# Kernel tuning notes

Measured on AMD Instinct MI355X. Metric: run time of the kernel, lower is better.

The kernel has to match this reference:

```python
import jax, jax.numpy as jnp
import numpy as np
from jax import lax

B, C, K = 16, 320, 8  # batch, channels, template kernel size
EPS = 1e-12  # F.normalize eps


def _pool_to(x, k):
    # adaptive avg pool to (k, k); H, W are exact multiples of k here
    b, c, h, w = x.shape
    return x.reshape(b, c, k, h // k, k, w // k).mean(axis=(3, 5))


def _l2norm(x):
    # L2 normalize over channel dim (dim=1), matching F.normalize(p=2, dim=1)
    n = jnp.sqrt(jnp.sum(x * x, axis=1, keepdims=True))
    return x / jnp.maximum(n, EPS)


def _fusion(feats, w1, b1, w2, b2):
    # global avg pool -> 2-layer MLP score per template -> softmax -> weighted sum
    scores = jnp.concatenate(
        [jax.nn.relu(f.mean(axis=(2, 3)) @ w1 + b1) @ w2 + b2 for f in feats], axis=1
    )  # (B, 3)
    a = jax.nn.softmax(scores, axis=1)
    return sum(a[:, i, None, None, None] * feats[i] for i in range(3))


def _corr(template_kernel, search):
    # depthwise correlation + channel sum == per-sample VALID conv with a
    # single (1, C, K, K) kernel; vmap over batch
    tn = _l2norm(template_kernel)  # (B, C, K, K)
    sn = _l2norm(search)           # (B, C, H, W)

    def one(sb, tb):
        return lax.conv_general_dilated(
            sb[None], tb[None], (1, 1), 'VALID',
            dimension_numbers=('NCHW', 'OIHW', 'NCHW'))[0]  # (1, Ho, Wo)

    return jax.vmap(one)(sn, tn)  # (B, 1, Ho, Wo)


_SPECS = [
    ('t0_p3', (B, C, 32, 32)), ('t0_p4', (B, C, 16, 16)), ('t0_p5', (B, C, 8, 8)),
    ('t1_p3', (B, C, 32, 32)), ('t1_p4', (B, C, 16, 16)), ('t1_p5', (B, C, 8, 8)),
    ('t2_p3', (B, C, 32, 32)), ('t2_p4', (B, C, 16, 16)), ('t2_p5', (B, C, 8, 8)),
    ('s_p3', (B, C, 64, 64)), ('s_p4', (B, C, 32, 32)), ('s_p5', (B, C, 16, 16)),
]
_PARAMS = [
    ('fp3_w1', (C, C // 4)), ('fp3_b1', (C // 4,)), ('fp3_w2', (C // 4, 1)), ('fp3_b2', (1,)),
    ('fp4_w1', (C, C // 4)), ('fp4_b1', (C // 4,)), ('fp4_w2', (C // 4, 1)), ('fp4_b2', (1,)),
    ('fp5_w1', (C, C // 4)), ('fp5_b1', (C // 4,)), ('fp5_w2', (C // 4, 1)), ('fp5_b2', (1,)),
]


def setup_inputs() -> dict:
    key = jax.random.key(0)
    d = {}
    for i, (name, shape) in enumerate(_SPECS):
        d[name] = jax.random.normal(jax.random.fold_in(key, i), shape, jnp.float32)
    for j, (name, shape) in enumerate(_PARAMS):
        k = jax.random.fold_in(key, 100 + j)
        if name.endswith('b1') or name.endswith('b2'):
            d[name] = jnp.zeros(shape, jnp.float32)
        else:
            d[name] = jax.random.normal(k, shape, jnp.float32) * 0.05
    return d


def reference(t0_p3, t0_p4, t0_p5, t1_p3, t1_p4, t1_p5, t2_p3, t2_p4, t2_p5,
              s_p3, s_p4, s_p5,
              fp3_w1, fp3_b1, fp3_w2, fp3_b2,
              fp4_w1, fp4_b1, fp4_w2, fp4_b2,
              fp5_w1, fp5_b1, fp5_w2, fp5_b2):
    tp3 = _fusion([t0_p3, t1_p3, t2_p3], fp3_w1, fp3_b1, fp3_w2, fp3_b2)
    tp4 = _fusion([t0_p4, t1_p4, t2_p4], fp4_w1, fp4_b1, fp4_w2, fp4_b2)
    tp5 = _fusion([t0_p5, t1_p5, t2_p5], fp5_w1, fp5_b1, fp5_w2, fp5_b2)
    corr_p3 = _corr(_pool_to(tp3, K), s_p3)  # (B, 1, 57, 57)
    corr_p4 = _corr(_pool_to(tp4, K), s_p4)  # (B, 1, 25, 25)
    corr_p5 = _corr(_pool_to(tp5, K), s_p5)  # (B, 1, 9, 9)
    return (corr_p3, corr_p4, corr_p5)
```

## Files before the change

### kernel.cpp

```cpp
#include <hip/hip_runtime.h>
#include <math.h>

#define BATCH 16
#define CH 320

typedef __attribute__((ext_vector_type(8))) short bf16x8;
typedef __attribute__((ext_vector_type(4))) float f32x4;

union FragU { bf16x8 f; unsigned long long u[2]; };

static constexpr size_t PLSZ     = (size_t)BATCH * CH * 64;
static constexpr size_t WS_POOL3 = 0;
static constexpr size_t WS_POOL4 = 3 * PLSZ;
static constexpr size_t WS_TF    = 6 * PLSZ;
static constexpr size_t WS_MEANS = 9 * PLSZ;
static constexpr size_t WS_AW    = WS_MEANS + 9 * BATCH * CH;
static constexpr size_t WS_PART  = WS_AW + 144;
static constexpr size_t WS_ABF   = WS_PART + 3 * BATCH * 80 * 64;
static constexpr size_t UB3 = 0;
static constexpr size_t UB4 = (size_t)BATCH * 4096 * 64;
static constexpr size_t UB5 = UB4 + (size_t)BATCH * 1024 * 64;

__device__ __forceinline__ float bf2f(unsigned short u) {
    union { unsigned int i; float f; } x; x.i = ((unsigned int)u) << 16; return x.f;
}
__device__ __forceinline__ unsigned short f2bf(float f) {
    union { float f; unsigned int i; } x; x.f = f;
    return (unsigned short)((x.i + 0x7FFFu + ((x.i >> 16) & 1u)) >> 16);
}
__device__ __forceinline__ unsigned cvtpk(float lo, float hi) {
    unsigned r;
    asm("v_cvt_pk_bf16_f32 %0, %1, %2" : "=v"(r) : "v"(lo), "v"(hi));
    return r;
}

template <int HW, int KK>
__device__ __forceinline__ void pool_body(int idx, const float* __restrict__ a0,
                                          const float* __restrict__ a1, const float* __restrict__ a2,
                                          float* __restrict__ dst, float* __restrict__ means, int lane) {
    constexpr int NPL = BATCH * CH * 64;
    int tmpl = idx / NPL;
    int r = idx % NPL;
    const float* src = (tmpl == 0) ? a0 : ((tmpl == 1) ? a1 : a2);
    int bc = r >> 6;
    int pos = r & 63;
    int oh = pos >> 3, ow = pos & 7;
    const float* base = src + (size_t)bc * HW * HW;
    float s = 0.0f;
    if constexpr (KK == 4) {
#pragma unroll
        for (int i = 0; i < 4; ++i) {
            float4 v = *(const float4*)(base + (oh * 4 + i) * HW + ow * 4);
            s += v.x + v.y + v.z + v.w;
        }
    } else {
#pragma unroll
        for (int i = 0; i < 2; ++i) {
            float2 v = *(const float2*)(base + (oh * 2 + i) * HW + ow * 2);
            s += v.x + v.y;
        }
    }
    s *= (1.0f / (KK * KK));
    dst[idx] = s;
    float m = s;
#pragma unroll
    for (int o = 32; o; o >>= 1) m += __shfl_xor(m, o);
    if (lane == 0) means[tmpl * (BATCH * CH) + bc] = m * (1.0f / 64.0f);
}

__global__ __launch_bounds__(256) void prep_kernel(
    const float* __restrict__ t0p3, const float* __restrict__ t1p3, const float* __restrict__ t2p3,
    const float* __restrict__ t0p4, const float* __restrict__ t1p4, const float* __restrict__ t2p4,
    const float* __restrict__ t0p5, const float* __restrict__ t1p5, const float* __restrict__ t2p5,
    float* __restrict__ pool3, float* __restrict__ pool4, float* __restrict__ means) {
    int bid = blockIdx.x, t = threadIdx.x, lane = t & 63;
    if (bid < 3840) {
        pool_body<32, 4>(bid * 256 + t, t0p3, t1p3, t2p3, pool3, means, lane);
    } else if (bid < 7680) {
        pool_body<16, 2>((bid - 3840) * 256 + t, t0p4, t1p4, t2p4, pool4, means + 3 * BATCH * CH, lane);
    } else {
        int w = ((bid - 7680) * 256 + t) >> 6;
        constexpr int NR = BATCH * CH;
        int tmpl = w / NR, rem = w % NR;
        const float* src = (tmpl == 0) ? t0p5 : ((tmpl == 1) ? t1p5 : t2p5);
        float v = src[(size_t)rem * 64 + lane];
#pragma unroll
        for (int o = 32; o; o >>= 1) v += __shfl_xor(v, o);
        if (lane == 0) means[6 * BATCH * CH + w] = v * (1.0f / 64.0f);
    }
}

__global__ __launch_bounds__(256) void weights_kernel(const float* __restrict__ means,
        const float* w13, const float* b13, const float* w23, const float* b23,
        const float* w14, const float* b14, const float* w24, const float* b24,
        const float* w15, const float* b15, const float* w25, const float* b25,
        float* __restrict__ a_out) {
    __shared__ float m[3 * CH];
    __shared__ float hv[240];
    __shared__ float sc[3];
    int lvl = blockIdx.x / BATCH;
    int b = blockIdx.x % BATCH;
    int t = threadIdx.x;
    const float* w1 = (lvl == 0) ? w13 : ((lvl == 1) ? w14 : w15);
    const float* b1 = (lvl == 0) ? b13 : ((lvl == 1) ? b14 : b15);
    const float* w2 = (lvl == 0) ? w23 : ((lvl == 1) ? w24 : w25);
    const float* b2 = (lvl == 0) ? b23 : ((lvl == 1) ? b24 : b25);
    const float* mb = means + lvl * (3 * BATCH * CH);
    for (int j = t; j < 3 * CH; j += 256) {
        int i = j / CH, c = j % CH;
        m[j] = mb[i * (BATCH * CH) + b * CH + c];
    }
    __syncthreads();
    if (t < 240) {
        int i = t / 80, jj = t % 80;
        float acc = b1[jj];
#pragma unroll 4
        for (int c = 0; c < CH; ++c) acc = fmaf(m[i * CH + c], w1[c * 80 + jj], acc);
        hv[t] = fmaxf(acc, 0.0f) * w2[jj];
    }
    __syncthreads();
    if (t < 3) {
        float s = b2[0];
#pragma unroll 8
        for (int jj = 0; jj < 80; ++jj) s += hv[t * 80 + jj];
        sc[t] = s;
    }
    __syncthreads();
    if (t == 0) {
        float mx = fmaxf(sc[0], fmaxf(sc[1], sc[2]));
        float e0 = expf(sc[0] - mx), e1 = expf(sc[1] - mx), e2 = expf(sc[2] - mx);
        float inv = 1.0f / (e0 + e1 + e2);
        float* ao = a_out + lvl * 48 + b * 3;
        ao[0] = e0 * inv; ao[1] = e1 * inv; ao[2] = e2 * inv;
    }
}

__global__ __launch_bounds__(256) void fuse_kernel(
        const float* __restrict__ p30, const float* __restrict__ p31, const float* __restrict__ p32,
        const float* __restrict__ p40, const float* __restrict__ p41, const float* __restrict__ p42,
        const float* __restrict__ p50, const float* __restrict__ p51, const float* __restrict__ p52,
        const float* __restrict__ aw, float* __restrict__ tf, float* __restrict__ partial) {
    __shared__ float red[256];
    int lvl = blockIdx.x / 1280;
    int r = blockIdx.x % 1280;
    int t = threadIdx.x;
    const float* p0 = (lvl == 0) ? p30 : ((lvl == 1) ? p40 : p50);
    const float* p1 = (lvl == 0) ? p31 : ((lvl == 1) ? p41 : p51);
    const float* p2 = (lvl == 0) ? p32 : ((lvl == 1) ? p42 : p52);
    int idx = r * 256 + t;
    int b = r / 80;
    int j = r % 80;
    const float* ab = aw + lvl * 48 + b * 3;
    float a0 = ab[0], a1 = ab[1], a2 = ab[2];
    float v = a0 * p0[idx] + a1 * p1[idx] + a2 * p2[idx];
    tf[(size_t)lvl * PLSZ + idx] = v;
    red[t] = v * v;
    __syncthreads();
    if (t < 64) {
        float s = red[t] + red[t + 64] + red[t + 128] + red[t + 192];
        partial[((size_t)(lvl * BATCH + b) * 80 + j) * 64 + t] = s;
    }
}

__global__ __launch_bounds__(256) void atrans_kernel(const float* __restrict__ tf,
        const float* __restrict__ part, short* __restrict__ abf) {
    __shared__ float lds[64 * 68];
    __shared__ float red2[4 * 64];
    __shared__ float sv[64];
    int lvl = blockIdx.x >> 4;
    int b = blockIdx.x & 15;
    int t = threadIdx.x;
    {
        const float* p = part + ((size_t)(lvl * BATCH + b) * 80) * 64 + (t & 63);
        int jg = t >> 6;
        float s = 0.0f;
        for (int j = jg * 20; j < jg * 20 + 20; ++j) s += p[j * 64];
        red2[jg * 64 + (t & 63)] = s;
    }
    __syncthreads();
    if (t < 64) {
        float s = red2[t] + red2[64 + t] + red2[128 + t] + red2[192 + t];
        sv[t] = 1.0f / fmaxf(sqrtf(s), 1e-12f);
    }
    __syncthreads();
    const float* tb = tf + (size_t)lvl * PLSZ + (size_t)b * (CH * 64);
    short* ab = abf + ((size_t)(lvl * BATCH + b) * 64) * 320;
    for (int c0 = 0; c0 < 320; c0 += 64) {
        __syncthreads();
#pragma unroll
        for (int i = 0; i < 4; ++i) {
            int c = (t >> 4) + 16 * i;
            int p4 = (t & 15) * 4;
            *(float4*)(lds + c * 68 + p4) = *(const float4*)(tb + (size_t)(c0 + c) * 64 + p4);
        }
        __syncthreads();
        int p = t >> 2;
        int cs = (t & 3) * 16;
        float s_p = sv[p];
        bf16x8 o0, o1;
#pragma unroll
        for (int u = 0; u < 8; ++u) o0[u] = (short)f2bf(lds[(cs + u) * 68 + p] * s_p);
#pragma unroll
        for (int u = 0; u < 8; ++u) o1[u] = (short)f2bf(lds[(cs + 8 + u) * 68 + p] * s_p);
        *(bf16x8*)(ab + (size_t)p * 320 + c0 + cs) = o0;
        *(bf16x8*)(ab + (size_t)p * 320 + c0 + cs + 8) = o1;
    }
}

template <int H>
__device__ __forceinline__ void gemm_body(const float* __restrict__ S, const short* __restrict__ T,
                                          short* __restrict__ V, int bid,
                                          unsigned short* St, float* red, float* invs) {
    constexpr int N = H * H;
    constexpr int XB = N / 64;
    int b = bid / XB;
    int x0b = (bid % XB) * 64;
    int t = threadIdx.x;
    int w = t >> 6, l = t & 63, g = l >> 4, ln = l & 15;
    int cg = t >> 4;
    int x0 = (t & 15) * 4;

    const float* Sb = S + (size_t)b * CH * N + x0b;
    const short* Tp = T + ((size_t)b * 64 + 16 * w + ln) * 320 + 8 * g;

    f32x4 acc[4];
#pragma unroll
    for (int i = 0; i < 4; ++i) acc[i] = (f32x4){0.f, 0.f, 0.f, 0.f};
    float ssq[4] = {0.f, 0.f, 0.f, 0.f};

    unsigned trbase = (unsigned)(size_t)St + (unsigned)(g * 256 + ln * 8);
    int e1 = ((x0 >> 4) * 8 + (cg >> 2)) * 64 + (cg & 3) * 16 + (x0 & 15);

    {
        const float* p = Sb + (size_t)cg * N + x0;
        float4 v1 = *(const float4*)(p);
        float4 v2 = *(const float4*)(p + (size_t)16 * N);
        ssq[0] = fmaf(v1.x, v1.x, fmaf(v2.x, v2.x, ssq[0]));
        ssq[1] = fmaf(v1.y, v1.y, fmaf(v2.y, v2.y, ssq[1]));
        ssq[2] = fmaf(v1.z, v1.z, fmaf(v2.z, v2.z, ssq[2]));
        ssq[3] = fmaf(v1.w, v1.w, fmaf(v2.w, v2.w, ssq[3]));
        *(uint2*)(St + e1)       = (uint2){cvtpk(v1.x, v1.y), cvtpk(v1.z, v1.w)};
        *(uint2*)(St + e1 + 256) = (uint2){cvtpk(v2.x, v2.y), cvtpk(v2.z, v2.w)};
    }
    bf16x8 tcur = *(const bf16x8*)(Tp);
    __syncthreads();

#define TRRD2(FR, OFF) \
    asm volatile("ds_read_b64_tr_b16 %0, %2 offset:%c3\n\tds_read_b64_tr_b16 %1, %2 offset:%c4" \
                 : "=v"((FR).u[0]), "=v"((FR).u[1]) : "v"(trbase), "i"(OFF), "i"((OFF) + 128));

#define GSTEP(BUF, S_) { \
    int kn = 32 * ((S_) + 1); \
    bool dost = kn < 320; \
    int kl = dost ? kn : 288; \
    const float* p_ = Sb + (size_t)(kl + cg) * N + x0; \
    float4 v1 = *(const float4*)(p_); \
    float4 v2 = *(const float4*)(p_ + (size_t)16 * N); \
    bf16x8 tnx = *(const bf16x8*)(Tp + kl); \
    FragU fr0, fr1, fr2, fr3; \
    TRRD2(fr0, (BUF) * 4096 + 0) \
    TRRD2(fr1, (BUF) * 4096 + 1024) \
    TRRD2(fr2, (BUF) * 4096 + 2048) \
    TRRD2(fr3, (BUF) * 4096 + 3072) \
    asm volatile("s_waitcnt lgkmcnt(0)" ::: "memory"); \
    __builtin_amdgcn_sched_barrier(0); \
    acc[0] = __builtin_amdgcn_mfma_f32_16x16x32_bf16(fr0.f, tcur, acc[0], 0, 0, 0); \
    acc[1] = __builtin_amdgcn_mfma_f32_16x16x32_bf16(fr1.f, tcur, acc[1], 0, 0, 0); \
    acc[2] = __builtin_amdgcn_mfma_f32_16x16x32_bf16(fr2.f, tcur, acc[2], 0, 0, 0); \
    acc[3] = __builtin_amdgcn_mfma_f32_16x16x32_bf16(fr3.f, tcur, acc[3], 0, 0, 0); \
    if (dost) { \
        ssq[0] = fmaf(v1.x, v1.x, fmaf(v2.x, v2.x, ssq[0])); \
        ssq[1] = fmaf(v1.y, v1.y, fmaf(v2.y, v2.y, ssq[1])); \
        ssq[2] = fmaf(v1.z, v1.z, fmaf(v2.z, v2.z, ssq[2])); \
        ssq[3] = fmaf(v1.w, v1.w, fmaf(v2.w, v2.w, ssq[3])); \
        unsigned short* d_ = St + (((BUF) ^ 1) * 2048) + e1; \
        *(uint2*)(d_)       = (uint2){cvtpk(v1.x, v1.y), cvtpk(v1.z, v1.w)}; \
        *(uint2*)(d_ + 256) = (uint2){cvtpk(v2.x, v2.y), cvtpk(v2.z, v2.w)}; \
    } \
    tcur = tnx; \
    __syncthreads(); }

    for (int s = 0; s < 10; s += 2) {
        GSTEP(0, s)
        GSTEP(1, s + 1)
    }
#undef GSTEP
#undef TRRD2

    *(f32x4*)(red + cg * 64 + x0) = (f32x4){ssq[0], ssq[1], ssq[2], ssq[3]};
    __syncthreads();
    if (t < 64) {
        float s = 0.0f;
#pragma unroll
        for (int i = 0; i < 16; ++i) s += red[i * 64 + t];
        invs[t] = 1.0f / fmaxf(sqrtf(s), 1e-12f);
    }
    __syncthreads();

    short* Vb = V + ((size_t)b * N + x0b) * 64 + 16 * w + ln;
#pragma unroll
    for (int mt = 0; mt < 4; ++mt) {
        f32x4 iv = *(f32x4*)(invs + mt * 16 + 4 * g);
#pragma unroll
        for (int r = 0; r < 4; ++r)
            Vb[(size_t)(mt * 16 + 4 * g + r) * 64] = (short)f2bf(acc[mt][r] * iv[r]);
    }
}

__global__ __launch_bounds__(256) void gemm_kernel(const float* __restrict__ sp3,
        const float* __restrict__ sp4, const float* __restrict__ sp5,
        const short* __restrict__ abf, short* __restrict__ u) {
    __shared__ unsigned short St[2 * 2048];
    __shared__ float red[16 * 64];
    __shared__ float invs[64];
    int bid = blockIdx.x;
    if (bid < 1024)      gemm_body<64>(sp3, abf,          u + UB3, bid,        St, red, invs);
    else if (bid < 1280) gemm_body<32>(sp4, abf + 327680, u + UB4, bid - 1024, St, red, invs);
    else                 gemm_body<16>(sp5, abf + 655360, u + UB5, bid - 1280, St, red, invs);
}

__global__ __launch_bounds__(256) void combine_kernel(const short* __restrict__ U,
                                                      float* __restrict__ out) {
    int tid = blockIdx.x * 256 + threadIdx.x;
    if (tid < 51984) {
        int b = tid / 3249, r = tid % 3249;
        int oh = r / 57, ow = r % 57;
        const short* u = U + UB3 + ((size_t)b * 4096 + oh * 64 + ow) * 64;
        float s = 0.0f;
#pragma unroll
        for (int kh = 0; kh < 8; ++kh)
#pragma unroll
            for (int kw = 0; kw < 8; ++kw)
                s += bf2f((unsigned short)u[(kh * 64 + kw) * 64 + kh * 8 + kw]);
        out[tid] = s;
    } else if (tid < 61984) {
        int x = tid - 51984;
        int b = x / 625, r = x % 625;
        int oh = r / 25, ow = r % 25;
        const short* u = U + UB4 + ((size_t)b * 1024 + oh * 32 + ow) * 64;
        float s = 0.0f;
#pragma unroll
        for (int kh = 0; kh < 8; ++kh)
#pragma unroll
            for (int kw = 0; kw < 8; ++kw)
                s += bf2f((unsigned short)u[(kh * 32 + kw) * 64 + kh * 8 + kw]);
        out[tid] = s;
    } else if (tid < 63280) {
        int x = tid - 61984;
        int b = x / 81, r = x % 81;
        int oh = r / 9, ow = r % 9;
        const short* u = U + UB5 + ((size_t)b * 256 + oh * 16 + ow) * 64;
        float s = 0.0f;
#pragma unroll
        for (int kh = 0; kh < 8; ++kh)
#pragma unroll
            for (int kw = 0; kw < 8; ++kw)
                s += bf2f((unsigned short)u[(kh * 16 + kw) * 64 + kh * 8 + kw]);
        out[tid] = s;
    }
}

extern "C" void kernel_launch(void* const* d_in, const int* in_sizes, int n_in,
                              void* d_out, int out_size, void* d_ws, size_t ws_size,
                              hipStream_t stream) {
    const float* t0p3 = (const float*)d_in[0];
    const float* t0p4 = (const float*)d_in[1];
    const float* t0p5 = (const float*)d_in[2];
    const float* t1p3 = (const float*)d_in[3];
    const float* t1p4 = (const float*)d_in[4];
    const float* t1p5 = (const float*)d_in[5];
    const float* t2p3 = (const float*)d_in[6];
    const float* t2p4 = (const float*)d_in[7];
    const float* t2p5 = (const float*)d_in[8];
    const float* sp3  = (const float*)d_in[9];
    const float* sp4  = (const float*)d_in[10];
    const float* sp5  = (const float*)d_in[11];
    const float* f3w1 = (const float*)d_in[12];
    const float* f3b1 = (const float*)d_in[13];
    const float* f3w2 = (const float*)d_in[14];
    const float* f3b2 = (const float*)d_in[15];
    const float* f4w1 = (const float*)d_in[16];
    const float* f4b1 = (const float*)d_in[17];
    const float* f4w2 = (const float*)d_in[18];
    const float* f4b2 = (const float*)d_in[19];
    const float* f5w1 = (const float*)d_in[20];
    const float* f5b1 = (const float*)d_in[21];
    const float* f5w2 = (const float*)d_in[22];
    const float* f5b2 = (const float*)d_in[23];

    float* ws = (float*)d_ws;
    short* abf = (short*)(ws + WS_ABF);
    short* ubuf = (short*)ws;

    prep_kernel<<<11520, 256, 0, stream>>>(t0p3, t1p3, t2p3, t0p4, t1p4, t2p4,
                                           t0p5, t1p5, t2p5,
                                           ws + WS_POOL3, ws + WS_POOL4, ws + WS_MEANS);
    weights_kernel<<<48, 256, 0, stream>>>(ws + WS_MEANS,
                                           f3w1, f3b1, f3w2, f3b2,
                                           f4w1, f4b1, f4w2, f4b2,
                                           f5w1, f5b1, f5w2, f5b2, ws + WS_AW);
    fuse_kernel<<<3840, 256, 0, stream>>>(ws + WS_POOL3, ws + WS_POOL3 + PLSZ, ws + WS_POOL3 + 2 * PLSZ,
                                          ws + WS_POOL4, ws + WS_POOL4 + PLSZ, ws + WS_POOL4 + 2 * PLSZ,
                                          t0p5, t1p5, t2p5,
                                          ws + WS_AW, ws + WS_TF, ws + WS_PART);
    atrans_kernel<<<48, 256, 0, stream>>>(ws + WS_TF, ws + WS_PART, abf);
    gemm_kernel<<<1344, 256, 0, stream>>>(sp3, sp4, sp5, abf, ubuf);
    combine_kernel<<<248, 256, 0, stream>>>(ubuf, (float*)d_out);
}
```

Before: 89.38 us.

## Deepen global prefetch to three stages in search GEMM and raise MFMA priority

The search-feature GEMM loop now keeps global loads three K-steps ahead in a register ring instead of one, fully unrolls the ten steps, and moves the LDS store of the next tile before the wait so it overlaps the fragment reads. It wraps the MFMA block in s_setprio and replaces __syncthreads with raw s_barrier after an explicit lgkmcnt wait. Launch bounds now request four waves per SIMD. The aim is to hide HBM latency in a memory-bound loop, at the cost of more registers, which the occupancy hint may force into spills.

```diff
diff --git a/kernel.cpp b/kernel.cpp
--- a/kernel.cpp
+++ b/kernel.cpp
@@ -213,6 +213,8 @@
                                           unsigned short* St, float* red, float* invs) {
     constexpr int N = H * H;
     constexpr int XB = N / 64;
+    constexpr int NSTEP = 10;
+    constexpr int DEPTH = 3;
     int b = bid / XB;
     int x0b = (bid % XB) * 64;
     int t = threadIdx.x;
@@ -220,7 +222,7 @@
     int cg = t >> 4;
     int x0 = (t & 15) * 4;
 
-    const float* Sb = S + (size_t)b * CH * N + x0b;
+    const float* Sp = S + (size_t)b * CH * N + x0b + (size_t)cg * N + x0;
     const short* Tp = T + ((size_t)b * 64 + 16 * w + ln) * 320 + 8 * g;
 
     f32x4 acc[4];
@@ -231,61 +233,69 @@
     unsigned trbase = (unsigned)(size_t)St + (unsigned)(g * 256 + ln * 8);
     int e1 = ((x0 >> 4) * 8 + (cg >> 2)) * 64 + (cg & 3) * 16 + (x0 & 15);
 
+    float4 pv1[DEPTH], pv2[DEPTH];
+    bf16x8 ptf[DEPTH];
+#pragma unroll
+    for (int s = 0; s < DEPTH; ++s) {
+        const float* p = Sp + (size_t)(32 * s) * N;
+        pv1[s] = *(const float4*)(p);
+        pv2[s] = *(const float4*)(p + (size_t)16 * N);
+        ptf[s] = *(const bf16x8*)(Tp + 32 * s);
+    }
+
+#define SSQ_ACC(V1, V2) \
+    ssq[0] = fmaf((V1).x, (V1).x, fmaf((V2).x, (V2).x, ssq[0])); \
+    ssq[1] = fmaf((V1).y, (V1).y, fmaf((V2).y, (V2).y, ssq[1])); \
+    ssq[2] = fmaf((V1).z, (V1).z, fmaf((V2).z, (V2).z, ssq[2])); \
+    ssq[3] = fmaf((V1).w, (V1).w, fmaf((V2).w, (V2).w, ssq[3]));
+
     {
-        const float* p = Sb + (size_t)cg * N + x0;
-        float4 v1 = *(const float4*)(p);
-        float4 v2 = *(const float4*)(p + (size_t)16 * N);
-        ssq[0] = fmaf(v1.x, v1.x, fmaf(v2.x, v2.x, ssq[0]));
-        ssq[1] = fmaf(v1.y, v1.y, fmaf(v2.y, v2.y, ssq[1]));
-        ssq[2] = fmaf(v1.z, v1.z, fmaf(v2.z, v2.z, ssq[2]));
-        ssq[3] = fmaf(v1.w, v1.w, fmaf(v2.w, v2.w, ssq[3]));
+        float4 v1 = pv1[0], v2 = pv2[0];
+        SSQ_ACC(v1, v2)
         *(uint2*)(St + e1)       = (uint2){cvtpk(v1.x, v1.y), cvtpk(v1.z, v1.w)};
         *(uint2*)(St + e1 + 256) = (uint2){cvtpk(v2.x, v2.y), cvtpk(v2.z, v2.w)};
     }
-    bf16x8 tcur = *(const bf16x8*)(Tp);
-    __syncthreads();
+    asm volatile("s_waitcnt lgkmcnt(0)" ::: "memory");
+    __builtin_amdgcn_s_barrier();
 
 #define TRRD2(FR, OFF) \
     asm volatile("ds_read_b64_tr_b16 %0, %2 offset:%c3\n\tds_read_b64_tr_b16 %1, %2 offset:%c4" \
                  : "=v"((FR).u[0]), "=v"((FR).u[1]) : "v"(trbase), "i"(OFF), "i"((OFF) + 128));
 
-#define GSTEP(BUF, S_) { \
-    int kn = 32 * ((S_) + 1); \
-    bool dost = kn < 320; \
-    int kl = dost ? kn : 288; \
-    const float* p_ = Sb + (size_t)(kl + cg) * N + x0; \
-    float4 v1 = *(const float4*)(p_); \
-    float4 v2 = *(const float4*)(p_ + (size_t)16 * N); \
-    bf16x8 tnx = *(const bf16x8*)(Tp + kl); \
-    FragU fr0, fr1, fr2, fr3; \
-    TRRD2(fr0, (BUF) * 4096 + 0) \
-    TRRD2(fr1, (BUF) * 4096 + 1024) \
-    TRRD2(fr2, (BUF) * 4096 + 2048) \
-    TRRD2(fr3, (BUF) * 4096 + 3072) \
-    asm volatile("s_waitcnt lgkmcnt(0)" ::: "memory"); \
-    __builtin_amdgcn_sched_barrier(0); \
-    acc[0] = __builtin_amdgcn_mfma_f32_16x16x32_bf16(fr0.f, tcur, acc[0], 0, 0, 0); \
-    acc[1] = __builtin_amdgcn_mfma_f32_16x16x32_bf16(fr1.f, tcur, acc[1], 0, 0, 0); \
-    acc[2] = __builtin_amdgcn_mfma_f32_16x16x32_bf16(fr2.f, tcur, acc[2], 0, 0, 0); \
-    acc[3] = __builtin_amdgcn_mfma_f32_16x16x32_bf16(fr3.f, tcur, acc[3], 0, 0, 0); \
-    if (dost) { \
-        ssq[0] = fmaf(v1.x, v1.x, fmaf(v2.x, v2.x, ssq[0])); \
-        ssq[1] = fmaf(v1.y, v1.y, fmaf(v2.y, v2.y, ssq[1])); \
-        ssq[2] = fmaf(v1.z, v1.z, fmaf(v2.z, v2.z, ssq[2])); \
-        ssq[3] = fmaf(v1.w, v1.w, fmaf(v2.w, v2.w, ssq[3])); \
-        unsigned short* d_ = St + (((BUF) ^ 1) * 2048) + e1; \
-        *(uint2*)(d_)       = (uint2){cvtpk(v1.x, v1.y), cvtpk(v1.z, v1.w)}; \
-        *(uint2*)(d_ + 256) = (uint2){cvtpk(v2.x, v2.y), cvtpk(v2.z, v2.w)}; \
-    } \
-    tcur = tnx; \
-    __syncthreads(); }
-
-    for (int s = 0; s < 10; s += 2) {
-        GSTEP(0, s)
-        GSTEP(1, s + 1)
-    }
-#undef GSTEP
+#pragma unroll
+    for (int s = 0; s < NSTEP; ++s) {
+        const int cur = s & 1;
+        bf16x8 tcur = ptf[s % DEPTH];
+        if (s + DEPTH < NSTEP) {
+            const float* p = Sp + (size_t)(32 * (s + DEPTH)) * N;
+            pv1[(s + DEPTH) % DEPTH] = *(const float4*)(p);
+            pv2[(s + DEPTH) % DEPTH] = *(const float4*)(p + (size_t)16 * N);
+            ptf[(s + DEPTH) % DEPTH] = *(const bf16x8*)(Tp + 32 * (s + DEPTH));
+        }
+        FragU fr0, fr1, fr2, fr3;
+        TRRD2(fr0, cur * 4096 + 0)
+        TRRD2(fr1, cur * 4096 + 1024)
+        TRRD2(fr2, cur * 4096 + 2048)
+        TRRD2(fr3, cur * 4096 + 3072)
+        if (s + 1 < NSTEP) {
+            float4 v1 = pv1[(s + 1) % DEPTH], v2 = pv2[(s + 1) % DEPTH];
+            SSQ_ACC(v1, v2)
+            unsigned short* d_ = St + ((cur ^ 1) * 2048) + e1;
+            *(uint2*)(d_)       = (uint2){cvtpk(v1.x, v1.y), cvtpk(v1.z, v1.w)};
+            *(uint2*)(d_ + 256) = (uint2){cvtpk(v2.x, v2.y), cvtpk(v2.z, v2.w)};
+        }
+        asm volatile("s_waitcnt lgkmcnt(0)" ::: "memory");
+        __builtin_amdgcn_sched_barrier(0);
+        __builtin_amdgcn_s_setprio(1);
+        acc[0] = __builtin_amdgcn_mfma_f32_16x16x32_bf16(fr0.f, tcur, acc[0], 0, 0, 0);
+        acc[1] = __builtin_amdgcn_mfma_f32_16x16x32_bf16(fr1.f, tcur, acc[1], 0, 0, 0);
+        acc[2] = __builtin_amdgcn_mfma_f32_16x16x32_bf16(fr2.f, tcur, acc[2], 0, 0, 0);
+        acc[3] = __builtin_amdgcn_mfma_f32_16x16x32_bf16(fr3.f, tcur, acc[3], 0, 0, 0);
+        __builtin_amdgcn_s_setprio(0);
+        __builtin_amdgcn_s_barrier();
+    }
 #undef TRRD2
+#undef SSQ_ACC
 
     *(f32x4*)(red + cg * 64 + x0) = (f32x4){ssq[0], ssq[1], ssq[2], ssq[3]};
     __syncthreads();
@@ -307,7 +317,7 @@
     }
 }
 
-__global__ __launch_bounds__(256) void gemm_kernel(const float* __restrict__ sp3,
+__global__ __launch_bounds__(256, 4) void gemm_kernel(const float* __restrict__ sp3,
         const float* __restrict__ sp4, const float* __restrict__ sp5,
         const short* __restrict__ abf, short* __restrict__ u) {
     __shared__ unsigned short St[2 * 2048];
```

Measured after the change: 95.01 us. 1.06x slower.

## Load GEMM operands straight from global memory, removing LDS staging and block syncs

Applied to the files above, without the earlier changes.

The search-feature GEMM no longer stages converted bf16 tiles in LDS with transpose reads and double buffering. Each wave now loads its own 16 spatial columns of fp32 data from global memory, converts them to a bf16 A fragment in registers, and loads template B fragments directly. The channel-norm reduction moves from an LDS tree with block barriers to wave shuffles, and the operand roles are swapped so the output store layout changes. This removes LDS traffic and __syncthreads and raises the occupancy hint. The cost is strided, less coalesced global loads (8 channel rows per lane) and repeated template fragment loads per wave.

```diff
diff --git a/kernel.cpp b/kernel.cpp
--- a/kernel.cpp
+++ b/kernel.cpp
@@ -7,7 +7,7 @@
 typedef __attribute__((ext_vector_type(8))) short bf16x8;
 typedef __attribute__((ext_vector_type(4))) float f32x4;
 
-union FragU { bf16x8 f; unsigned long long u[2]; };
+union AFrag { bf16x8 f; unsigned q[4]; };
 
 static constexpr size_t PLSZ     = (size_t)BATCH * CH * 64;
 static constexpr size_t WS_POOL3 = 0;
@@ -209,114 +209,68 @@
 
 template <int H>
 __device__ __forceinline__ void gemm_body(const float* __restrict__ S, const short* __restrict__ T,
-                                          short* __restrict__ V, int bid,
-                                          unsigned short* St, float* red, float* invs) {
+                                          short* __restrict__ V, int bid) {
     constexpr int N = H * H;
     constexpr int XB = N / 64;
     int b = bid / XB;
     int x0b = (bid % XB) * 64;
     int t = threadIdx.x;
     int w = t >> 6, l = t & 63, g = l >> 4, ln = l & 15;
-    int cg = t >> 4;
-    int x0 = (t & 15) * 4;
-
-    const float* Sb = S + (size_t)b * CH * N + x0b;
-    const short* Tp = T + ((size_t)b * 64 + 16 * w + ln) * 320 + 8 * g;
+    int xw = x0b + 16 * w;
+
+    const float* Sb = S + (size_t)b * CH * N + xw + ln;
+    const short* Tb = T + (size_t)b * 64 * 320;
 
     f32x4 acc[4];
 #pragma unroll
     for (int i = 0; i < 4; ++i) acc[i] = (f32x4){0.f, 0.f, 0.f, 0.f};
-    float ssq[4] = {0.f, 0.f, 0.f, 0.f};
-
-    unsigned trbase = (unsigned)(size_t)St + (unsigned)(g * 256 + ln * 8);
-    int e1 = ((x0 >> 4) * 8 + (cg >> 2)) * 64 + (cg & 3) * 16 + (x0 & 15);
-
-    {
-        const float* p = Sb + (size_t)cg * N + x0;
-        float4 v1 = *(const float4*)(p);
-        float4 v2 = *(const float4*)(p + (size_t)16 * N);
-        ssq[0] = fmaf(v1.x, v1.x, fmaf(v2.x, v2.x, ssq[0]));
-        ssq[1] = fmaf(v1.y, v1.y, fmaf(v2.y, v2.y, ssq[1]));
-        ssq[2] = fmaf(v1.z, v1.z, fmaf(v2.z, v2.z, ssq[2]));
-        ssq[3] = fmaf(v1.w, v1.w, fmaf(v2.w, v2.w, ssq[3]));
-        *(uint2*)(St + e1)       = (uint2){cvtpk(v1.x, v1.y), cvtpk(v1.z, v1.w)};
-        *(uint2*)(St + e1 + 256) = (uint2){cvtpk(v2.x, v2.y), cvtpk(v2.z, v2.w)};
-    }
-    bf16x8 tcur = *(const bf16x8*)(Tp);
-    __syncthreads();
-
-#define TRRD2(FR, OFF) \
-    asm volatile("ds_read_b64_tr_b16 %0, %2 offset:%c3\n\tds_read_b64_tr_b16 %1, %2 offset:%c4" \
-                 : "=v"((FR).u[0]), "=v"((FR).u[1]) : "v"(trbase), "i"(OFF), "i"((OFF) + 128));
-
-#define GSTEP(BUF, S_) { \
-    int kn = 32 * ((S_) + 1); \
-    bool dost = kn < 320; \
-    int kl = dost ? kn : 288; \
-    const float* p_ = Sb + (size_t)(kl + cg) * N + x0; \
-    float4 v1 = *(const float4*)(p_); \
-    float4 v2 = *(const float4*)(p_ + (size_t)16 * N); \
-    bf16x8 tnx = *(const bf16x8*)(Tp + kl); \
-    FragU fr0, fr1, fr2, fr3; \
-    TRRD2(fr0, (BUF) * 4096 + 0) \
-    TRRD2(fr1, (BUF) * 4096 + 1024) \
-    TRRD2(fr2, (BUF) * 4096 + 2048) \
-    TRRD2(fr3, (BUF) * 4096 + 3072) \
-    asm volatile("s_waitcnt lgkmcnt(0)" ::: "memory"); \
-    __builtin_amdgcn_sched_barrier(0); \
-    acc[0] = __builtin_amdgcn_mfma_f32_16x16x32_bf16(fr0.f, tcur, acc[0], 0, 0, 0); \
-    acc[1] = __builtin_amdgcn_mfma_f32_16x16x32_bf16(fr1.f, tcur, acc[1], 0, 0, 0); \
-    acc[2] = __builtin_amdgcn_mfma_f32_16x16x32_bf16(fr2.f, tcur, acc[2], 0, 0, 0); \
-    acc[3] = __builtin_amdgcn_mfma_f32_16x16x32_bf16(fr3.f, tcur, acc[3], 0, 0, 0); \
-    if (dost) { \
-        ssq[0] = fmaf(v1.x, v1.x, fmaf(v2.x, v2.x, ssq[0])); \
-        ssq[1] = fmaf(v1.y, v1.y, fmaf(v2.y, v2.y, ssq[1])); \
-        ssq[2] = fmaf(v1.z, v1.z, fmaf(v2.z, v2.z, ssq[2])); \
-        ssq[3] = fmaf(v1.w, v1.w, fmaf(v2.w, v2.w, ssq[3])); \
-        unsigned short* d_ = St + (((BUF) ^ 1) * 2048) + e1; \
-        *(uint2*)(d_)       = (uint2){cvtpk(v1.x, v1.y), cvtpk(v1.z, v1.w)}; \
-        *(uint2*)(d_ + 256) = (uint2){cvtpk(v2.x, v2.y), cvtpk(v2.z, v2.w)}; \
-    } \
-    tcur = tnx; \
-    __syncthreads(); }
-
-    for (int s = 0; s < 10; s += 2) {
-        GSTEP(0, s)
-        GSTEP(1, s + 1)
-    }
-#undef GSTEP
-#undef TRRD2
-
-    *(f32x4*)(red + cg * 64 + x0) = (f32x4){ssq[0], ssq[1], ssq[2], ssq[3]};
-    __syncthreads();
-    if (t < 64) {
-        float s = 0.0f;
-#pragma unroll
-        for (int i = 0; i < 16; ++i) s += red[i * 64 + t];
-        invs[t] = 1.0f / fmaxf(sqrtf(s), 1e-12f);
-    }
-    __syncthreads();
-
-    short* Vb = V + ((size_t)b * N + x0b) * 64 + 16 * w + ln;
-#pragma unroll
-    for (int mt = 0; mt < 4; ++mt) {
-        f32x4 iv = *(f32x4*)(invs + mt * 16 + 4 * g);
+    float ssq = 0.0f;
+
+#pragma unroll
+    for (int s = 0; s < 10; ++s) {
+        int c0 = 32 * s + 8 * g;
+        float av[8];
+#pragma unroll
+        for (int j = 0; j < 8; ++j) av[j] = Sb[(size_t)(c0 + j) * N];
+        bf16x8 tb0 = *(const bf16x8*)(Tb + (size_t)(0 * 16 + ln) * 320 + c0);
+        bf16x8 tb1 = *(const bf16x8*)(Tb + (size_t)(1 * 16 + ln) * 320 + c0);
+        bf16x8 tb2 = *(const bf16x8*)(Tb + (size_t)(2 * 16 + ln) * 320 + c0);
+        bf16x8 tb3 = *(const bf16x8*)(Tb + (size_t)(3 * 16 + ln) * 320 + c0);
+#pragma unroll
+        for (int j = 0; j < 8; ++j) ssq = fmaf(av[j], av[j], ssq);
+        AFrag fa;
+        fa.q[0] = cvtpk(av[0], av[1]);
+        fa.q[1] = cvtpk(av[2], av[3]);
+        fa.q[2] = cvtpk(av[4], av[5]);
+        fa.q[3] = cvtpk(av[6], av[7]);
+        acc[0] = __builtin_amdgcn_mfma_f32_16x16x32_bf16(fa.f, tb0, acc[0], 0, 0, 0);
+        acc[1] = __builtin_amdgcn_mfma_f32_16x16x32_bf16(fa.f, tb1, acc[1], 0, 0, 0);
+        acc[2] = __builtin_amdgcn_mfma_f32_16x16x32_bf16(fa.f, tb2, acc[2], 0, 0, 0);
+        acc[3] = __builtin_amdgcn_mfma_f32_16x16x32_bf16(fa.f, tb3, acc[3], 0, 0, 0);
+    }
+
+    ssq += __shfl_xor(ssq, 16);
+    ssq += __shfl_xor(ssq, 32);
+    float inv = 1.0f / fmaxf(sqrtf(ssq), 1e-12f);
+    float iv[4];
+#pragma unroll
+    for (int r = 0; r < 4; ++r) iv[r] = __shfl(inv, 4 * g + r);
+
+#pragma unroll
+    for (int pt = 0; pt < 4; ++pt)
 #pragma unroll
         for (int r = 0; r < 4; ++r)
-            Vb[(size_t)(mt * 16 + 4 * g + r) * 64] = (short)f2bf(acc[mt][r] * iv[r]);
-    }
-}
-
-__global__ __launch_bounds__(256) void gemm_kernel(const float* __restrict__ sp3,
+            V[((size_t)b * N + xw + 4 * g + r) * 64 + pt * 16 + ln] =
+                (short)f2bf(acc[pt][r] * iv[r]);
+}
+
+__global__ __launch_bounds__(256, 4) void gemm_kernel(const float* __restrict__ sp3,
         const float* __restrict__ sp4, const float* __restrict__ sp5,
         const short* __restrict__ abf, short* __restrict__ u) {
-    __shared__ unsigned short St[2 * 2048];
-    __shared__ float red[16 * 64];
-    __shared__ float invs[64];
     int bid = blockIdx.x;
-    if (bid < 1024)      gemm_body<64>(sp3, abf,          u + UB3, bid,        St, red, invs);
-    else if (bid < 1280) gemm_body<32>(sp4, abf + 327680, u + UB4, bid - 1024, St, red, invs);
-    else                 gemm_body<16>(sp5, abf + 655360, u + UB5, bid - 1280, St, red, invs);
+    if (bid < 1024)      gemm_body<64>(sp3, abf,          u + UB3, bid);
+    else if (bid < 1280) gemm_body<32>(sp4, abf + 327680, u + UB4, bid - 1024);
+    else                 gemm_body<16>(sp5, abf + 655360, u + UB5, bid - 1280);
 }
 
 __global__ __launch_bounds__(256) void combine_kernel(const short* __restrict__ U,
```

Measured after the change: 99.82 us. +11.7%, slower.
